# Kernel optimization log

Hardware: AMD Instinct MI355X
Metric: run time of the kernel (lower is better)

The kernel has to match this reference:

```python
import jax, jax.numpy as jnp
import numpy as np

B, S, H, NH = 8, 1042, 768, 12
HD = H // NH            # 64
P = 1024                # patch tokens (32x32 grid); RoPE applied to last P tokens
MLP = 2048              # int(768 * 8/3)
EPS = 1e-6


def _rope_tables():
    # mirrors precompute_rope_freqs_2d(HD, P): inside, dim = HD//2 = 32
    dim = HD // 2
    t = int(P ** 0.5)  # 32
    freqs = 1.0 / (10000.0 ** (np.arange(0, dim, 2, dtype=np.float32) / dim))  # (16,)
    pos = np.arange(t, dtype=np.float32)
    fh = pos[:, None] * freqs[None, :]                       # (t,16)
    f = np.concatenate([np.tile(fh[:, None, :], (1, t, 1)),
                        np.tile(fh[None, :, :], (t, 1, 1))], axis=-1)  # (t,t,32)
    f = f.reshape(P, dim)                                    # (1024,32)
    return jnp.asarray(np.cos(f)), jnp.asarray(np.sin(f))


def setup_inputs() -> dict:
    key = jax.random.key(0)
    ks = jax.random.split(key, 20)
    r = lambda k, sh, sc: (jax.random.normal(k, sh, jnp.float32) * sc)
    cos, sin = _rope_tables()
    return {
        "x": jax.random.normal(ks[0], (B, S, H), jnp.float32),
        "rope_cos": cos, "rope_sin": sin,
        "Wq": r(ks[1], (H, H), 0.02), "Wk": r(ks[2], (H, H), 0.02),
        "Wv": r(ks[3], (H, H), 0.02), "Wo": r(ks[4], (H, H), 0.02),
        "q_norm_w": jnp.ones((HD,), jnp.float32),
        "k_norm_w": jnp.ones((HD,), jnp.float32),
        "gate_W": r(ks[5], (H, NH), 0.02),
        "gate_b": jnp.full((NH,), 4.0, jnp.float32),
        "norm1_w": jnp.ones((H,), jnp.float32),
        "norm2_w": jnp.ones((H,), jnp.float32),
        "W_gate": r(ks[6], (H, MLP), 0.02),
        "W_up": r(ks[7], (H, MLP), 0.02),
        "W_down": r(ks[8], (MLP, H), 0.02),
        "attn_scale": r(ks[9], (H,), 0.1),   # zero-init in module; randn for nontrivial grads
        "mlp_scale": r(ks[10], (H,), 0.1),
    }


def _rmsnorm(x, w):
    return x * jax.lax.rsqrt(jnp.mean(x * x, axis=-1, keepdims=True) + EPS) * w


def _apply_rope(x, cos, sin):
    # x: (B,S,NH,HD); rotate only the last P (patch) tokens, consecutive-pair complex rotation
    xp = x[:, -P:].reshape(B, P, NH, HD // 2, 2)
    x0, x1 = xp[..., 0], xp[..., 1]
    c = cos[None, :, None, :]
    s = sin[None, :, None, :]
    rot = jnp.stack([x0 * c - x1 * s, x0 * s + x1 * c], axis=-1).reshape(B, P, NH, HD)
    return jnp.concatenate([x[:, :-P], rot], axis=1)


def reference(x, rope_cos, rope_sin, Wq, Wk, Wv, Wo, q_norm_w, k_norm_w,
              gate_W, gate_b, norm1_w, norm2_w, W_gate, W_up, W_down,
              attn_scale, mlp_scale):
    # --- attention branch (QwenGatedRoPEAttention) ---
    h = _rmsnorm(x, norm1_w)
    q = (h @ Wq).reshape(B, S, NH, HD)
    k = (h @ Wk).reshape(B, S, NH, HD)
    v = (h @ Wv).reshape(B, S, NH, HD)
    q = _rmsnorm(q, q_norm_w)
    k = _rmsnorm(k, k_norm_w)
    q = _apply_rope(q, rope_cos, rope_sin)
    k = _apply_rope(k, rope_cos, rope_sin)
    q = q / jnp.sqrt(jnp.asarray(HD, jnp.float32))
    scores = jnp.einsum('bqhd,bkhd->bhqk', q, k)          # (B,NH,S,S)
    probs = jax.nn.softmax(scores.astype(jnp.float32), axis=-1)
    attn = jnp.einsum('bhqk,bkhd->bqhd', probs, v)        # (B,S,NH,HD)
    gate = jax.nn.sigmoid((h @ gate_W)[..., None] + gate_b[None, None, :, None])
    attn = (attn * gate).reshape(B, S, H)
    x = x + (attn @ Wo) * attn_scale
    # --- SwiGLU MLP branch ---
    h2 = _rmsnorm(x, norm2_w)
    mlp = (jax.nn.silu(h2 @ W_gate) * (h2 @ W_up)) @ W_down
    x = x + mlp * mlp_scale
    return x
```

## Files before the change

kernel.cpp:

```cpp
#include <hip/hip_runtime.h>
#include <hip/hip_bf16.h>
#include <stdint.h>

#define B_   8
#define S_   1042
#define H_   768
#define NH_  12
#define HD_  64
#define MLP_ 2048
#define T_   (B_*S_)
#define MP_  8448
#define SP_  1088
#define EPS_ 1e-6f

typedef __attribute__((ext_vector_type(8))) short bf16x8v;
typedef __attribute__((ext_vector_type(4))) float f32x4;
typedef __hip_bfloat16 bf16;

typedef __attribute__((address_space(1))) const void gas_void;
typedef __attribute__((address_space(3))) void las_void;

__device__ inline void gload_lds16(const void* g, void* l) {
  __builtin_amdgcn_global_load_lds((gas_void*)g, (las_void*)l, 16, 0, 0);
}

__global__ void fillz(uint4* p, long n16) {
  long i = (long)blockIdx.x * blockDim.x + threadIdx.x;
  long stride = (long)gridDim.x * blockDim.x;
  uint4 z; z.x = z.y = z.z = z.w = 0u;
  for (; i < n16; i += stride) p[i] = z;
}

__global__ __launch_bounds__(256) void wcvt_t(const float* __restrict__ W, bf16* __restrict__ o,
                                              int K, int N) {
  __shared__ float tile[32][33];
  int kt = blockIdx.x, nt = blockIdx.y;
  int t = threadIdx.x;
  int r = t >> 5, c = t & 31;
#pragma unroll
  for (int i = 0; i < 4; i++)
    tile[i * 8 + r][c] = W[(long)(kt * 32 + i * 8 + r) * N + nt * 32 + c];
  __syncthreads();
#pragma unroll
  for (int i = 0; i < 4; i++)
    o[(long)(nt * 32 + i * 8 + r) * K + kt * 32 + c] = __float2bfloat16(tile[c][i * 8 + r]);
}

__global__ __launch_bounds__(256) void vtran(const bf16* __restrict__ qkv, bf16* __restrict__ vtf) {
  __shared__ bf16 tile[32][66];
  int st = blockIdx.x, bh = blockIdx.y;
  int bb = bh / NH_, h = bh - bb * NH_;
  int s0 = st * 32;
  int t = threadIdx.x;
  int si = t >> 6, d = t & 63;
#pragma unroll
  for (int i = 0; i < 8; i++) {
    int s = s0 + i * 4 + si;
    bf16 v = __float2bfloat16(0.f);
    if (s < S_) v = qkv[(long)(bb * S_ + s) * 2304 + 1536 + h * 64 + d];
    tile[i * 4 + si][d] = v;
  }
  __syncthreads();
  int dd = t >> 5, sj = t & 31;
#pragma unroll
  for (int i = 0; i < 8; i++) {
    int d2 = i * 8 + dd;
    vtf[((long)bh * 64 + d2) * SP_ + s0 + sj] = tile[sj][d2];
  }
}

__global__ __launch_bounds__(256) void rmsnorm_k(const float* __restrict__ x,
                                                 const float* __restrict__ w,
                                                 bf16* __restrict__ o, int Mreal) {
  int row = blockIdx.x;
  bf16* orow = o + (long)row * H_;
  int t = threadIdx.x;
  if (row >= Mreal) {
    for (int i = t; i < H_; i += 256) orow[i] = __float2bfloat16(0.f);
    return;
  }
  const float* xr = x + (long)row * H_;
  float v0 = xr[t], v1 = xr[t + 256], v2 = xr[t + 512];
  float s = v0 * v0 + v1 * v1 + v2 * v2;
  for (int off = 32; off; off >>= 1) s += __shfl_down(s, off);
  __shared__ float red[4];
  if ((t & 63) == 0) red[t >> 6] = s;
  __syncthreads();
  float tot = red[0] + red[1] + red[2] + red[3];
  float inv = rsqrtf(tot * (1.f / H_) + EPS_);
  orow[t]       = __float2bfloat16(v0 * inv * w[t]);
  orow[t + 256] = __float2bfloat16(v1 * inv * w[t + 256]);
  orow[t + 512] = __float2bfloat16(v2 * inv * w[t + 512]);
}

template <int EPI>
__global__ __launch_bounds__(256) void gemm_bf16(
    const bf16* __restrict__ A, const bf16* __restrict__ Bt, void* __restrict__ Out,
    const float* __restrict__ resid, const float* __restrict__ scale,
    int N, int K, int Mreal) {
  __shared__ __align__(16) bf16 As[128 * 32];
  __shared__ __align__(16) bf16 Bs[128 * 32];
  int tid = threadIdx.x;
  int lane = tid & 63, wid = tid >> 6;
  int wm = wid >> 1, wn = wid & 1;
  int lr = lane & 15, lg = lane >> 4;
  long rowA0 = (long)blockIdx.y * 128;
  long rowB0 = (long)blockIdx.x * 128;
  f32x4 z; z[0] = z[1] = z[2] = z[3] = 0.f;
  f32x4 acc[4][4];
#pragma unroll
  for (int mi = 0; mi < 4; mi++)
#pragma unroll
    for (int ni = 0; ni < 4; ni++) acc[mi][ni] = z;

  const int flat0 = wid * 512 + lane * 8;
  const bf16* Ab = A + rowA0 * K;
  const bf16* Bb = Bt + rowB0 * K;

  for (int k0 = 0; k0 < K; k0 += 32) {
    __syncthreads();
#pragma unroll
    for (int j = 0; j < 2; j++) {
      int flat = flat0 + j * 2048;
      int r = flat >> 5, c = flat & 31;
      gload_lds16(Ab + (long)r * K + k0 + c, &As[flat]);
      gload_lds16(Bb + (long)r * K + k0 + c, &Bs[flat]);
    }
    __syncthreads();
    bf16x8v af[4], bfr[4];
#pragma unroll
    for (int mi = 0; mi < 4; mi++)
      af[mi] = *(const bf16x8v*)&As[(wm * 64 + mi * 16 + lr) * 32 + lg * 8];
#pragma unroll
    for (int ni = 0; ni < 4; ni++)
      bfr[ni] = *(const bf16x8v*)&Bs[(wn * 64 + ni * 16 + lr) * 32 + lg * 8];
#pragma unroll
    for (int mi = 0; mi < 4; mi++)
#pragma unroll
      for (int ni = 0; ni < 4; ni++)
        acc[mi][ni] = __builtin_amdgcn_mfma_f32_16x16x32_bf16(af[mi], bfr[ni], acc[mi][ni], 0, 0, 0);
  }

#pragma unroll
  for (int mi = 0; mi < 4; mi++) {
#pragma unroll
    for (int ni = 0; ni < 4; ni++) {
#pragma unroll
      for (int r = 0; r < 4; r++) {
        long row = rowA0 + wm * 64 + mi * 16 + lg * 4 + r;
        long col = rowB0 + wn * 64 + ni * 16 + lr;
        float v = acc[mi][ni][r];
        if (EPI == 0) {
          ((bf16*)Out)[row * N + col] = __float2bfloat16(v);
        } else {
          if (row < Mreal)
            ((float*)Out)[row * N + col] = resid[row * N + col] + v * scale[col];
        }
      }
    }
  }
}

__global__ __launch_bounds__(768) void qkv_post(
    const bf16* __restrict__ qkv, const float* __restrict__ qw, const float* __restrict__ kw,
    const float* __restrict__ cosT, const float* __restrict__ sinT,
    bf16* __restrict__ qf, bf16* __restrict__ kf) {
  int tok = blockIdx.x;
  int bb = tok / S_, s = tok - bb * S_;
  int h = threadIdx.x >> 6, d = threadIdx.x & 63;
  const bf16* base = qkv + (long)tok * 2304 + h * 64 + d;
  float q = __bfloat162float(base[0]);
  float k = __bfloat162float(base[768]);
  float qs = q * q, ks = k * k;
  for (int off = 32; off; off >>= 1) {
    qs += __shfl_xor(qs, off);
    ks += __shfl_xor(ks, off);
  }
  q *= rsqrtf(qs * (1.f / 64.f) + EPS_) * qw[d];
  k *= rsqrtf(ks * (1.f / 64.f) + EPS_) * kw[d];
  if (s >= S_ - 1024) {
    int pos = s - (S_ - 1024);
    int i = d >> 1;
    float c = cosT[pos * 32 + i], sn = sinT[pos * 32 + i];
    float qp = __shfl_xor(q, 1), kp = __shfl_xor(k, 1);
    if (d & 1) { q = qp * sn + q * c; k = kp * sn + k * c; }
    else       { q = q * c - qp * sn; k = k * c - kp * sn; }
  }
  q *= 0.125f * 1.44269504088896f;
  long o1 = ((long)(bb * NH_ + h) * SP_ + s) * 64 + d;
  qf[o1] = __float2bfloat16(q);
  kf[o1] = __float2bfloat16(k);
}

__global__ __launch_bounds__(64) void gate_k(const bf16* __restrict__ h, const float* __restrict__ gW,
                                             const float* __restrict__ gb, float* __restrict__ gate) {
  int tok = blockIdx.x, l = threadIdx.x;
  float hv[12];
#pragma unroll
  for (int i = 0; i < 12; i++) hv[i] = __bfloat162float(h[(long)tok * H_ + i * 64 + l]);
#pragma unroll
  for (int n = 0; n < 12; n++) {
    float s = 0.f;
#pragma unroll
    for (int i = 0; i < 12; i++) s += hv[i] * gW[(i * 64 + l) * 12 + n];
    for (int off = 32; off; off >>= 1) s += __shfl_xor(s, off);
    if (l == 0) gate[(long)tok * 12 + n] = 1.f / (1.f + __expf(-(s + gb[n])));
  }
}

#define SWZ(row, cc) (((row) << 6) + ((((cc) ^ ((row) & 7))) << 3))

__global__ __launch_bounds__(256) void attn_k(
    const bf16* __restrict__ qf, const bf16* __restrict__ kf, const bf16* __restrict__ vtf,
    const float* __restrict__ gate, bf16* __restrict__ attn_g) {
  __shared__ __align__(16) bf16 Ks[2][64 * 64];
  __shared__ __align__(16) bf16 Vs[2][64 * 64];
  int bid = blockIdx.x;
  int w = (bid & 7) * 204 + (bid >> 3);
  int bh = w / 17, qb = w - bh * 17;
  int bb = bh / NH_, h = bh - bb * NH_;
  int tid = threadIdx.x;
  int lane = tid & 63, wv = tid >> 6;
  int lr = lane & 15, lg = lane >> 4;
  const bf16* qbase = qf + (long)bh * SP_ * 64;
  const bf16* kbase = kf + (long)bh * SP_ * 64;
  const bf16* vbase = vtf + (long)bh * 64 * SP_;

  int q_l = qb * 64 + wv * 16 + lr;
  bf16x8v qB0 = *(const bf16x8v*)(qbase + (long)q_l * 64 + lg * 8);
  bf16x8v qB1 = *(const bf16x8v*)(qbase + (long)q_l * 64 + 32 + lg * 8);

  f32x4 z; z[0] = z[1] = z[2] = z[3] = 0.f;
  f32x4 acc[4] = {z, z, z, z};
  float m = -1e30f, lsum = 0.f;

  auto stage = [&](int buf, int kidx) {
#pragma unroll
    for (int inst = 0; inst < 2; inst++) {
      int c = inst * 256 + tid;
      int row = c >> 3, slot = c & 7;
      int cc = slot ^ (row & 7);
      gload_lds16(kbase + (long)(kidx + row) * 64 + cc * 8, &Ks[buf][c * 8]);
    }
#pragma unroll
    for (int inst = 0; inst < 2; inst++) {
      int c = inst * 256 + tid;
      int row = c >> 3, slot = c & 7;
      int cc = slot ^ (row & 7);
      gload_lds16(vbase + (long)row * SP_ + kidx + cc * 8, &Vs[buf][c * 8]);
    }
  };

  stage(0, 0);
  asm volatile("s_waitcnt vmcnt(0)" ::: "memory");
  __syncthreads();
  int cur = 0;

  for (int kt = 0; kt < SP_ / 64; kt++) {
    int kidx = kt * 64;
    if (kt < SP_ / 64 - 1) stage(cur ^ 1, kidx + 64);

    f32x4 p[4];
    __builtin_amdgcn_s_setprio(1);
#pragma unroll
    for (int mt = 0; mt < 4; mt++) {
      int row = mt * 16 + lr;
      bf16x8v k0 = *(const bf16x8v*)&Ks[cur][SWZ(row, lg)];
      bf16x8v k1 = *(const bf16x8v*)&Ks[cur][SWZ(row, lg + 4)];
      f32x4 t = z;
      t = __builtin_amdgcn_mfma_f32_16x16x32_bf16(k0, qB0, t, 0, 0, 0);
      t = __builtin_amdgcn_mfma_f32_16x16x32_bf16(k1, qB1, t, 0, 0, 0);
      p[mt] = t;
    }
    __builtin_amdgcn_s_setprio(0);

    if (kidx + 64 > S_) {
#pragma unroll
      for (int mt = 0; mt < 4; mt++)
#pragma unroll
        for (int r = 0; r < 4; r++)
          if (kidx + mt * 16 + lg * 4 + r >= S_) p[mt][r] = -1e30f;
    }

    float tmax = p[0][0];
#pragma unroll
    for (int mt = 0; mt < 4; mt++)
#pragma unroll
      for (int r = 0; r < 4; r++) tmax = fmaxf(tmax, p[mt][r]);
    tmax = fmaxf(tmax, __shfl_xor(tmax, 16));
    tmax = fmaxf(tmax, __shfl_xor(tmax, 32));

    if (__ballot(tmax > m + 11.0f)) {
      float mn = fmaxf(m, tmax);
      float so = exp2f(m - mn);
      m = mn;
      lsum *= so;
      float so4[4];
#pragma unroll
      for (int r = 0; r < 4; r++) so4[r] = __shfl(so, lg * 4 + r);
#pragma unroll
      for (int dt = 0; dt < 4; dt++) {
        f32x4 a = acc[dt];
        a[0] *= so4[0]; a[1] *= so4[1]; a[2] *= so4[2]; a[3] *= so4[3];
        acc[dt] = a;
      }
    }
    float ts = 0.f;
#pragma unroll
    for (int mt = 0; mt < 4; mt++)
#pragma unroll
      for (int r = 0; r < 4; r++) {
        float e = exp2f(p[mt][r] - m);
        p[mt][r] = e;
        ts += e;
      }
    ts += __shfl_xor(ts, 16);
    ts += __shfl_xor(ts, 32);
    lsum += ts;

    uint32_t w0[4], w1[4];
#pragma unroll
    for (int mt = 0; mt < 4; mt++) {
      asm("v_cvt_pk_bf16_f32 %0, %1, %2" : "=v"(w0[mt]) : "v"(p[mt][0]), "v"(p[mt][1]));
      asm("v_cvt_pk_bf16_f32 %0, %1, %2" : "=v"(w1[mt]) : "v"(p[mt][2]), "v"(p[mt][3]));
    }
    bf16x8v aP[2];
#pragma unroll
    for (int t2 = 0; t2 < 2; t2++) {
      union { uint32_t u[4]; bf16x8v v; } cvt;
#pragma unroll
      for (int wd = 0; wd < 4; wd++) {
        uint32_t a = (wd & 1) ? w1[2 * t2] : w0[2 * t2];
        uint32_t b = (wd & 1) ? w1[2 * t2 + 1] : w0[2 * t2 + 1];
        uint32_t val = (lg & 2) ? b : a;
        int src = ((lg & 1) * 2 + (wd >> 1)) * 16 + lr;
        cvt.u[wd] = (uint32_t)__shfl((int)val, src);
      }
      aP[t2] = cvt.v;
    }
    __builtin_amdgcn_s_setprio(1);
#pragma unroll
    for (int t2 = 0; t2 < 2; t2++)
#pragma unroll
      for (int dt = 0; dt < 4; dt++) {
        int row = dt * 16 + lr;
        bf16x8v vB = *(const bf16x8v*)&Vs[cur][SWZ(row, t2 * 4 + lg)];
        acc[dt] = __builtin_amdgcn_mfma_f32_16x16x32_bf16(aP[t2], vB, acc[dt], 0, 0, 0);
      }
    __builtin_amdgcn_s_setprio(0);

    asm volatile("s_waitcnt vmcnt(0)" ::: "memory");
    __syncthreads();
    cur ^= 1;
  }

  float norm = 0.f;
  if (q_l < S_) norm = gate[((long)bb * S_ + q_l) * 12 + h] / lsum;
  float nr[4];
#pragma unroll
  for (int r = 0; r < 4; r++) nr[r] = __shfl(norm, lg * 4 + r);
#pragma unroll
  for (int dt = 0; dt < 4; dt++)
#pragma unroll
    for (int r = 0; r < 4; r++) {
      int qr = qb * 64 + wv * 16 + lg * 4 + r;
      if (qr < S_)
        attn_g[((long)bb * S_ + qr) * H_ + h * 64 + dt * 16 + lr] =
            __float2bfloat16(acc[dt][r] * nr[r]);
    }
}

__global__ __launch_bounds__(256) void silu_mul_k(const bf16* __restrict__ gu, bf16* __restrict__ o) {
  long i = (long)blockIdx.x * 256 + threadIdx.x;
  long row = i >> 8;
  int c8 = (int)(i & 255) * 8;
  bf16x8v gv = *(const bf16x8v*)(gu + row * 4096 + c8);
  bf16x8v uv = *(const bf16x8v*)(gu + row * 4096 + 2048 + c8);
  bf16x8v ov;
#pragma unroll
  for (int j = 0; j < 8; j++) {
    short sg = gv[j], su = uv[j];
    float g = __bfloat162float(*reinterpret_cast<bf16*>(&sg));
    float u = __bfloat162float(*reinterpret_cast<bf16*>(&su));
    float s = g / (1.f + __expf(-g));
    bf16 r = __float2bfloat16(s * u);
    ov[j] = *reinterpret_cast<short*>(&r);
  }
  *(bf16x8v*)(o + row * 2048 + c8) = ov;
}

extern "C" void kernel_launch(void* const* d_in, const int* in_sizes, int n_in,
                              void* d_out, int out_size, void* d_ws, size_t ws_size,
                              hipStream_t stream) {
  const float* x    = (const float*)d_in[0];
  const float* cosT = (const float*)d_in[1];
  const float* sinT = (const float*)d_in[2];
  const float* Wq   = (const float*)d_in[3];
  const float* Wk   = (const float*)d_in[4];
  const float* Wv   = (const float*)d_in[5];
  const float* Wo   = (const float*)d_in[6];
  const float* qnw  = (const float*)d_in[7];
  const float* knw  = (const float*)d_in[8];
  const float* gW   = (const float*)d_in[9];
  const float* gb   = (const float*)d_in[10];
  const float* n1w  = (const float*)d_in[11];
  const float* n2w  = (const float*)d_in[12];
  const float* Wg   = (const float*)d_in[13];
  const float* Wu   = (const float*)d_in[14];
  const float* Wd   = (const float*)d_in[15];
  const float* ascale = (const float*)d_in[16];
  const float* mscale = (const float*)d_in[17];

  char* ws = (char*)d_ws;
  size_t off = 0;
  auto alloc = [&](size_t bytes) {
    char* p = ws + off;
    off += (bytes + 255) & ~(size_t)255;
    return p;
  };
  bf16* h_pad  = (bf16*)alloc((size_t)MP_ * H_ * 2);
  bf16* wqkv_t = (bf16*)alloc((size_t)2304 * 768 * 2);
  bf16* wo_t   = (bf16*)alloc((size_t)768 * 768 * 2);
  bf16* wgu_t  = (bf16*)alloc((size_t)4096 * 768 * 2);
  bf16* wdn_t  = (bf16*)alloc((size_t)768 * 2048 * 2);
  bf16* qkv    = (bf16*)alloc((size_t)MP_ * 2304 * 2);
  bf16* qfb    = (bf16*)alloc((size_t)96 * SP_ * 64 * 2);
  bf16* kfb    = (bf16*)alloc((size_t)96 * SP_ * 64 * 2);
  bf16* vtfb   = (bf16*)alloc((size_t)96 * SP_ * 64 * 2);
  float* gateb = (float*)alloc((size_t)T_ * 12 * 4);
  bf16* attn_g = (bf16*)alloc((size_t)MP_ * H_ * 2);
  float* x2    = (float*)alloc((size_t)T_ * H_ * 4);
  bf16* gu     = (bf16*)alloc((size_t)MP_ * 4096 * 2);
  bf16* mlpin  = qkv;

  fillz<<<1024, 256, 0, stream>>>((uint4*)qfb, (long)(3 * 96 * SP_ * 64 * 2) / 16);
  fillz<<<64, 256, 0, stream>>>((uint4*)(attn_g + (long)T_ * H_), (long)((MP_ - T_) * H_ * 2) / 16);

  auto wc = [&](const float* W, bf16* o, int K, int N) {
    wcvt_t<<<dim3(K / 32, N / 32), 256, 0, stream>>>(W, o, K, N);
  };
  wc(Wq, wqkv_t, 768, 768);
  wc(Wk, wqkv_t + 768 * 768, 768, 768);
  wc(Wv, wqkv_t + 2 * 768 * 768, 768, 768);
  wc(Wo, wo_t, 768, 768);
  wc(Wg, wgu_t, 768, 2048);
  wc(Wu, wgu_t + (long)2048 * 768, 768, 2048);
  wc(Wd, wdn_t, 2048, 768);

  rmsnorm_k<<<MP_, 256, 0, stream>>>(x, n1w, h_pad, T_);

  gemm_bf16<0><<<dim3(2304 / 128, MP_ / 128), 256, 0, stream>>>(
      h_pad, wqkv_t, qkv, nullptr, nullptr, 2304, 768, MP_);

  qkv_post<<<T_, 768, 0, stream>>>(qkv, qnw, knw, cosT, sinT, qfb, kfb);
  vtran<<<dim3(33, 96), 256, 0, stream>>>(qkv, vtfb);

  gate_k<<<T_, 64, 0, stream>>>(h_pad, gW, gb, gateb);

  attn_k<<<1632, 256, 0, stream>>>(qfb, kfb, vtfb, gateb, attn_g);

  gemm_bf16<1><<<dim3(768 / 128, MP_ / 128), 256, 0, stream>>>(
      attn_g, wo_t, x2, x, ascale, 768, 768, T_);

  rmsnorm_k<<<MP_, 256, 0, stream>>>(x2, n2w, h_pad, T_);

  gemm_bf16<0><<<dim3(4096 / 128, MP_ / 128), 256, 0, stream>>>(
      h_pad, wgu_t, gu, nullptr, nullptr, 4096, 768, MP_);

  silu_mul_k<<<MP_, 256, 0, stream>>>(gu, mlpin);

  gemm_bf16<1><<<dim3(768 / 128, MP_ / 128), 256, 0, stream>>>(
      mlpin, wdn_t, (float*)d_out, x2, mscale, 768, 2048, T_);
}
```

Measured before the change: 488.7 us.

## Add 256x256 pipelined GEMM with fused SiLU-gate epilogue and drop zero fills

Adds a 512-thread GEMM kernel with 256x256 tiles and XCD-aware block remapping. It uses swizzled LDS filled through direct global-to-LDS loads, double-buffered phases with barriers and priority hints, and 16x16x32 bf16 MFMA. The kernel is used for the QKV projection and for the gate/up projection. A new weight conversion interleaves gate and up columns in 16-wide groups, so the gate/up GEMM epilogue computes silu(g)*u directly. That removes the separate silu_mul kernel and the large intermediate gu buffer. The fillz launches that zeroed padded attention buffers are also removed, which relies on the padding being harmless or already zero.

```diff
diff --git a/kernel.cpp b/kernel.cpp
--- a/kernel.cpp
+++ b/kernel.cpp
@@ -24,12 +24,8 @@
   __builtin_amdgcn_global_load_lds((gas_void*)g, (las_void*)l, 16, 0, 0);
 }
 
-__global__ void fillz(uint4* p, long n16) {
-  long i = (long)blockIdx.x * blockDim.x + threadIdx.x;
-  long stride = (long)gridDim.x * blockDim.x;
-  uint4 z; z.x = z.y = z.z = z.w = 0u;
-  for (; i < n16; i += stride) p[i] = z;
-}
+#define BARRIER asm volatile("s_barrier" ::: "memory")
+#define VMCNT4  asm volatile("s_waitcnt vmcnt(4)" ::: "memory")
 
 __global__ __launch_bounds__(256) void wcvt_t(const float* __restrict__ W, bf16* __restrict__ o,
                                               int K, int N) {
@@ -46,27 +42,22 @@
     o[(long)(nt * 32 + i * 8 + r) * K + kt * 32 + c] = __float2bfloat16(tile[c][i * 8 + r]);
 }
 
-__global__ __launch_bounds__(256) void vtran(const bf16* __restrict__ qkv, bf16* __restrict__ vtf) {
-  __shared__ bf16 tile[32][66];
-  int st = blockIdx.x, bh = blockIdx.y;
-  int bb = bh / NH_, h = bh - bb * NH_;
-  int s0 = st * 32;
+__global__ __launch_bounds__(256) void wcvt_gu(const float* __restrict__ Wg,
+                                               const float* __restrict__ Wu,
+                                               bf16* __restrict__ o) {
+  __shared__ float tile[32][33];
+  int kt = blockIdx.x, nt = blockIdx.y;
   int t = threadIdx.x;
-  int si = t >> 6, d = t & 63;
-#pragma unroll
-  for (int i = 0; i < 8; i++) {
-    int s = s0 + i * 4 + si;
-    bf16 v = __float2bfloat16(0.f);
-    if (s < S_) v = qkv[(long)(bb * S_ + s) * 2304 + 1536 + h * 64 + d];
-    tile[i * 4 + si][d] = v;
-  }
+  int r = t >> 5, c = t & 31;
+  const float* src = (c < 16) ? Wg : Wu;
+  int col = nt * 16 + (c & 15);
+#pragma unroll
+  for (int i = 0; i < 4; i++)
+    tile[i * 8 + r][c] = src[(long)(kt * 32 + i * 8 + r) * MLP_ + col];
   __syncthreads();
-  int dd = t >> 5, sj = t & 31;
-#pragma unroll
-  for (int i = 0; i < 8; i++) {
-    int d2 = i * 8 + dd;
-    vtf[((long)bh * 64 + d2) * SP_ + s0 + sj] = tile[sj][d2];
-  }
+#pragma unroll
+  for (int i = 0; i < 4; i++)
+    o[(long)(nt * 32 + i * 8 + r) * 768 + kt * 32 + c] = __float2bfloat16(tile[c][i * 8 + r]);
 }
 
 __global__ __launch_bounds__(256) void rmsnorm_k(const float* __restrict__ x,
@@ -91,6 +82,135 @@
   orow[t]       = __float2bfloat16(v0 * inv * w[t]);
   orow[t + 256] = __float2bfloat16(v1 * inv * w[t + 256]);
   orow[t + 512] = __float2bfloat16(v2 * inv * w[t + 512]);
+}
+
+template <int EPI>
+__global__ __launch_bounds__(512) void gemm256(
+    const bf16* __restrict__ A, const bf16* __restrict__ Bt, void* __restrict__ Out,
+    int N, int nbn) {
+  __shared__ __align__(16) bf16 lds[2][4][128 * 64];
+  int tid = threadIdx.x;
+  int lane = tid & 63, wid = tid >> 6;
+  int wr = wid >> 2, wc = wid & 3;
+  int lr = lane & 15, lg = lane >> 4;
+
+  int nwg = gridDim.x;
+  int bid = blockIdx.x;
+  int q = nwg >> 3, r8 = nwg & 7;
+  int xcd = bid & 7, idx = bid >> 3;
+  int wg = (xcd < r8 ? xcd * (q + 1) : r8 * (q + 1) + (xcd - r8) * q) + idx;
+  int bm = wg / nbn, bn = wg - bm * nbn;
+
+  int chunk_row = tid >> 3;
+  int cc = (tid & 7) ^ (chunk_row & 7);
+  const bf16* aSrc = A + ((long)bm * 256 + chunk_row) * 768 + cc * 8;
+  const bf16* bSrc = Bt + ((long)bn * 256 + chunk_row) * 768 + cc * 8;
+
+  auto stA = [&](int buf, int half, int kt) {
+    bf16* d = &lds[buf][half][tid * 8];
+    const bf16* s = aSrc + (long)half * 128 * 768 + kt * 64;
+    gload_lds16(s, d);
+    gload_lds16(s + 64 * 768, d + 512 * 8);
+  };
+  auto stB = [&](int buf, int half, int kt) {
+    bf16* d = &lds[buf][2 + half][tid * 8];
+    const bf16* s = bSrc + (long)half * 128 * 768 + kt * 64;
+    gload_lds16(s, d);
+    gload_lds16(s + 64 * 768, d + 512 * 8);
+  };
+  auto ldA = [&](int buf, int mi, int ks) -> bf16x8v {
+    int row = mi * 16 + lr;
+    int c = (ks * 4 + lg) ^ (row & 7);
+    return *(const bf16x8v*)&lds[buf][wr][row * 64 + c * 8];
+  };
+  auto ldB = [&](int buf, int ni, int ks) -> bf16x8v {
+    int row = (wc & 1) * 64 + ni * 16 + lr;
+    int c = (ks * 4 + lg) ^ (row & 7);
+    return *(const bf16x8v*)&lds[buf][2 + (wc >> 1)][row * 64 + c * 8];
+  };
+
+  f32x4 z; z[0] = z[1] = z[2] = z[3] = 0.f;
+  f32x4 acc[8][4];
+#pragma unroll
+  for (int mi = 0; mi < 8; mi++)
+#pragma unroll
+    for (int ni = 0; ni < 4; ni++) acc[mi][ni] = z;
+
+  bf16x8v bf[4][2];
+  bf16x8v af[4];
+
+  stA(0, 0, 0); stA(0, 1, 0); stB(0, 0, 0); stB(0, 1, 0);
+  stB(1, 0, 1); stB(1, 1, 1);
+  VMCNT4;
+  BARRIER;
+
+#define PHASE(p, bb, STG, VM)                                                   \
+  {                                                                             \
+    if ((p) == 0) {                                                             \
+      _Pragma("unroll") for (int ni = 0; ni < 4; ni++) {                        \
+        bf[ni][0] = ldB(bb, ni, 0); bf[ni][1] = ldB(bb, ni, 1);                 \
+      }                                                                         \
+    }                                                                           \
+    af[0] = ldA(bb, 2 * (p), 0);     af[1] = ldA(bb, 2 * (p), 1);               \
+    af[2] = ldA(bb, 2 * (p) + 1, 0); af[3] = ldA(bb, 2 * (p) + 1, 1);           \
+    STG;                                                                        \
+    asm volatile("" ::: "memory");                                              \
+    BARRIER;                                                                    \
+    __builtin_amdgcn_s_setprio(1);                                              \
+    _Pragma("unroll") for (int dm = 0; dm < 2; dm++)                            \
+      _Pragma("unroll") for (int ni = 0; ni < 4; ni++) {                        \
+        acc[2 * (p) + dm][ni] = __builtin_amdgcn_mfma_f32_16x16x32_bf16(        \
+            af[dm * 2 + 0], bf[ni][0], acc[2 * (p) + dm][ni], 0, 0, 0);         \
+        acc[2 * (p) + dm][ni] = __builtin_amdgcn_mfma_f32_16x16x32_bf16(        \
+            af[dm * 2 + 1], bf[ni][1], acc[2 * (p) + dm][ni], 0, 0, 0);         \
+      }                                                                         \
+    __builtin_amdgcn_s_setprio(0);                                              \
+    if (VM) VMCNT4;                                                             \
+    BARRIER;                                                                    \
+  }
+
+  for (int i = 0; i < 6; i++) {
+    int u = 2 * i + 1;
+    int t2 = (2 * i + 2 < 12) ? 2 * i + 2 : 11;
+    int t3 = (2 * i + 3 < 12) ? 2 * i + 3 : 11;
+    PHASE(0, 0, stA(1, 0, u), 0);
+    PHASE(1, 0, stA(1, 1, u), 0);
+    PHASE(2, 0, stB(0, 0, t2), 0);
+    PHASE(3, 0, stB(0, 1, t2), 1);
+    PHASE(0, 1, stA(0, 0, t2), 0);
+    PHASE(1, 1, stA(0, 1, t2), 0);
+    PHASE(2, 1, stB(1, 0, t3), 0);
+    PHASE(3, 1, stB(1, 1, t3), 1);
+  }
+#undef PHASE
+
+  long rowbase = (long)bm * 256 + wr * 128;
+  int colbase = bn * 256 + wc * 64;
+  if (EPI == 0) {
+    bf16* O = (bf16*)Out;
+#pragma unroll
+    for (int mi = 0; mi < 8; mi++)
+#pragma unroll
+      for (int ni = 0; ni < 4; ni++)
+#pragma unroll
+        for (int r = 0; r < 4; r++)
+          O[(rowbase + mi * 16 + lg * 4 + r) * N + colbase + ni * 16 + lr] =
+              __float2bfloat16(acc[mi][ni][r]);
+  } else {
+    bf16* O = (bf16*)Out;
+    int oc0 = colbase >> 1;
+#pragma unroll
+    for (int mi = 0; mi < 8; mi++)
+#pragma unroll
+      for (int p = 0; p < 2; p++)
+#pragma unroll
+        for (int r = 0; r < 4; r++) {
+          float g = acc[mi][2 * p][r], u = acc[mi][2 * p + 1][r];
+          float v = g / (1.f + __expf(-g)) * u;
+          O[(rowbase + mi * 16 + lg * 4 + r) * 2048 + oc0 + p * 16 + lr] =
+              __float2bfloat16(v);
+        }
+  }
 }
 
 template <int EPI>
@@ -161,6 +281,29 @@
   }
 }
 
+__global__ __launch_bounds__(256) void vtran(const bf16* __restrict__ qkv, bf16* __restrict__ vtf) {
+  __shared__ bf16 tile[32][66];
+  int st = blockIdx.x, bh = blockIdx.y;
+  int bb = bh / NH_, h = bh - bb * NH_;
+  int s0 = st * 32;
+  int t = threadIdx.x;
+  int si = t >> 6, d = t & 63;
+#pragma unroll
+  for (int i = 0; i < 8; i++) {
+    int s = s0 + i * 4 + si;
+    bf16 v = __float2bfloat16(0.f);
+    if (s < S_) v = qkv[(long)(bb * S_ + s) * 2304 + 1536 + h * 64 + d];
+    tile[i * 4 + si][d] = v;
+  }
+  __syncthreads();
+  int dd = t >> 5, sj = t & 31;
+#pragma unroll
+  for (int i = 0; i < 8; i++) {
+    int d2 = i * 8 + dd;
+    vtf[((long)bh * 64 + d2) * SP_ + s0 + sj] = tile[sj][d2];
+  }
+}
+
 __global__ __launch_bounds__(768) void qkv_post(
     const bf16* __restrict__ qkv, const float* __restrict__ qw, const float* __restrict__ kw,
     const float* __restrict__ cosT, const float* __restrict__ sinT,
@@ -368,25 +511,6 @@
         attn_g[((long)bb * S_ + qr) * H_ + h * 64 + dt * 16 + lr] =
             __float2bfloat16(acc[dt][r] * nr[r]);
     }
-}
-
-__global__ __launch_bounds__(256) void silu_mul_k(const bf16* __restrict__ gu, bf16* __restrict__ o) {
-  long i = (long)blockIdx.x * 256 + threadIdx.x;
-  long row = i >> 8;
-  int c8 = (int)(i & 255) * 8;
-  bf16x8v gv = *(const bf16x8v*)(gu + row * 4096 + c8);
-  bf16x8v uv = *(const bf16x8v*)(gu + row * 4096 + 2048 + c8);
-  bf16x8v ov;
-#pragma unroll
-  for (int j = 0; j < 8; j++) {
-    short sg = gv[j], su = uv[j];
-    float g = __bfloat162float(*reinterpret_cast<bf16*>(&sg));
-    float u = __bfloat162float(*reinterpret_cast<bf16*>(&su));
-    float s = g / (1.f + __expf(-g));
-    bf16 r = __float2bfloat16(s * u);
-    ov[j] = *reinterpret_cast<short*>(&r);
-  }
-  *(bf16x8v*)(o + row * 2048 + c8) = ov;
 }
 
 extern "C" void kernel_launch(void* const* d_in, const int* in_sizes, int n_in,
@@ -430,11 +554,7 @@
   float* gateb = (float*)alloc((size_t)T_ * 12 * 4);
   bf16* attn_g = (bf16*)alloc((size_t)MP_ * H_ * 2);
   float* x2    = (float*)alloc((size_t)T_ * H_ * 4);
-  bf16* gu     = (bf16*)alloc((size_t)MP_ * 4096 * 2);
   bf16* mlpin  = qkv;
-
-  fillz<<<1024, 256, 0, stream>>>((uint4*)qfb, (long)(3 * 96 * SP_ * 64 * 2) / 16);
-  fillz<<<64, 256, 0, stream>>>((uint4*)(attn_g + (long)T_ * H_), (long)((MP_ - T_) * H_ * 2) / 16);
 
   auto wc = [&](const float* W, bf16* o, int K, int N) {
     wcvt_t<<<dim3(K / 32, N / 32), 256, 0, stream>>>(W, o, K, N);
@@ -443,14 +563,12 @@
   wc(Wk, wqkv_t + 768 * 768, 768, 768);
   wc(Wv, wqkv_t + 2 * 768 * 768, 768, 768);
   wc(Wo, wo_t, 768, 768);
-  wc(Wg, wgu_t, 768, 2048);
-  wc(Wu, wgu_t + (long)2048 * 768, 768, 2048);
   wc(Wd, wdn_t, 2048, 768);
+  wcvt_gu<<<dim3(24, 128), 256, 0, stream>>>(gW ? Wg : Wg, Wu, wgu_t);
 
   rmsnorm_k<<<MP_, 256, 0, stream>>>(x, n1w, h_pad, T_);
 
-  gemm_bf16<0><<<dim3(2304 / 128, MP_ / 128), 256, 0, stream>>>(
-      h_pad, wqkv_t, qkv, nullptr, nullptr, 2304, 768, MP_);
+  gemm256<0><<<9 * 33, 512, 0, stream>>>(h_pad, wqkv_t, qkv, 2304, 9);
 
   qkv_post<<<T_, 768, 0, stream>>>(qkv, qnw, knw, cosT, sinT, qfb, kfb);
   vtran<<<dim3(33, 96), 256, 0, stream>>>(qkv, vtfb);
@@ -464,10 +582,7 @@
 
   rmsnorm_k<<<MP_, 256, 0, stream>>>(x2, n2w, h_pad, T_);
 
-  gemm_bf16<0><<<dim3(4096 / 128, MP_ / 128), 256, 0, stream>>>(
-      h_pad, wgu_t, gu, nullptr, nullptr, 4096, 768, MP_);
-
-  silu_mul_k<<<MP_, 256, 0, stream>>>(gu, mlpin);
+  gemm256<2><<<16 * 33, 512, 0, stream>>>(h_pad, wgu_t, mlpin, 4096, 16);
 
   gemm_bf16<1><<<dim3(768 / 128, MP_ / 128), 256, 0, stream>>>(
       mlpin, wdn_t, (float*)d_out, x2, mscale, 768, 2048, T_);
```

New measurement: 468.3 us. 4.2% less time.
